# Kernel tuning notes

Hardware: AMD Instinct MI355X
Metric: run time of the kernel (lower is better)

## Reference

```python
import jax, jax.numpy as jnp
import numpy as np

B, D_IN, U, M = 8192, 512, 256, 50  # batch, input_size, num_units(=v_size), max_n_msgs


def _w(key, shape, scale=0.02):
    return (jax.random.normal(key, shape, dtype=jnp.float32) * scale)


def setup_inputs() -> dict:
    key = jax.random.key(0)
    ks = jax.random.split(key, 32)
    inp = {
        "X": jax.random.normal(ks[0], (B, D_IN), dtype=jnp.float32),
        "S": jax.random.normal(ks[1], (B, M, U), dtype=jnp.float32),
        "h": jax.random.normal(ks[2], (B, U), dtype=jnp.float32),
        "v": jax.random.normal(ks[3], (B, U), dtype=jnp.float32),
        # attention params
        "W_sa": _w(ks[4], (U, U)), "W_ha": _w(ks[5], (U, U)),
        "b_a": jnp.zeros((U,), jnp.float32), "v_a": _w(ks[6], (U,)),
        # gates
        "W_f": _w(ks[7], (U, U)), "W_hf": _w(ks[8], (U, U)), "b_f": jnp.zeros((U,), jnp.float32),
        "W_o": _w(ks[9], (U, U)), "W_ho": _w(ks[10], (U, U)), "b_o": jnp.zeros((U,), jnp.float32),
        "W_t": _w(ks[11], (U, U)), "W_ht": _w(ks[12], (U, U)), "b_t": jnp.zeros((U,), jnp.float32),
        "W_k": _w(ks[13], (D_IN, U)), "W_hk": _w(ks[14], (U, U)), "W_vk": _w(ks[15], (U, U)), "b_k": jnp.zeros((U,), jnp.float32),
        "W_s": _w(ks[16], (D_IN, U)), "W_hs": _w(ks[17], (U, U)), "b_s": jnp.zeros((U,), jnp.float32),
        "W_v": _w(ks[18], (U, U)), "W_hv": _w(ks[19], (U, U)), "b_v": jnp.zeros((U,), jnp.float32),
    }
    return inp


def reference(X, S, h, v,
              W_sa, W_ha, b_a, v_a,
              W_f, W_hf, b_f,
              W_o, W_ho, b_o,
              W_t, W_ht, b_t,
              W_k, W_hk, W_vk, b_k,
              W_s, W_hs, b_s,
              W_v, W_hv, b_v):
    # additive attention over messages: a [B, M, U]
    a = jnp.tanh(jnp.einsum('bmv,vu->bmu', S, W_sa) + (h @ W_ha + b_a)[:, None, :])
    scores = jnp.einsum('bmu,u->bm', a, v_a)            # [B, M]
    P = jax.nn.softmax(scores, axis=1)                  # [B, M]
    text = jnp.einsum('bm,bmv->bv', P, S)               # [B, U]
    # LSTM-like gates
    F = jax.nn.sigmoid(text @ W_f + h @ W_hf + b_f)
    O = jax.nn.sigmoid(text @ W_o + h @ W_ho + b_o)
    text_new = jnp.tanh(text @ W_t + h @ W_ht + b_t)
    V = F * v + O * text_new                            # [B, U]
    k = jax.nn.sigmoid(X @ W_k + h @ W_hk + V @ W_vk + b_k)
    hx = jnp.tanh(X @ W_s + h @ W_hs + b_s)
    hv = jnp.tanh(V @ W_v + h @ W_hv + b_v)
    H = (1.0 - k) * hv + k * hx                         # [B, U]
    # original returns (H, P, MSINStateTuple(H, V)); new_state.h == H
    return (H, P, V)
```

## Files before the change

kernel.cpp:

```cpp
#include <hip/hip_runtime.h>
#include <cstddef>

typedef __bf16 bf16x8 __attribute__((ext_vector_type(8)));
typedef unsigned short u16x8 __attribute__((ext_vector_type(8)));
typedef float f32x4 __attribute__((ext_vector_type(4)));

#define B_N 8192
#define M_N 50
#define R_N (B_N * M_N)
#define P_OFF ((size_t)B_N * 256)
#define V_OFF ((size_t)B_N * 256 + (size_t)B_N * 50)

__device__ __forceinline__ float bf2f(unsigned short u) {
  return __uint_as_float(((unsigned int)u) << 16);
}
__device__ __forceinline__ unsigned short f2bf(float f) {
  unsigned int u = __float_as_uint(f);
  u += 0x7fffu + ((u >> 16) & 1u);
  return (unsigned short)(u >> 16);
}
__device__ __forceinline__ float fsig(float x) { return 1.f / (1.f + __expf(-x)); }
__device__ __forceinline__ float ftanh(float x) {
  float e = __expf(2.f * x);
  return 1.f - 2.f / (e + 1.f);
}

__device__ __forceinline__ float ld_ext(const void* p, size_t i, bool f32) {
  return f32 ? ((const float*)p)[i] : bf2f(((const unsigned short*)p)[i]);
}
__device__ __forceinline__ void ld8_ext(unsigned short* dst, const void* p, size_t i, bool f32) {
  if (f32) {
    const float* fp = (const float*)p + i;
    const float4 a = *(const float4*)fp;
    const float4 b = *(const float4*)(fp + 4);
    u16x8 t;
    t[0] = f2bf(a.x); t[1] = f2bf(a.y); t[2] = f2bf(a.z); t[3] = f2bf(a.w);
    t[4] = f2bf(b.x); t[5] = f2bf(b.y); t[6] = f2bf(b.z); t[7] = f2bf(b.w);
    *(u16x8*)dst = t;
  } else {
    *(uint4*)dst = *(const uint4*)((const unsigned short*)p + i);
  }
}

__global__ void probe_dtype(const void* __restrict__ X, int* __restrict__ flag) {
  const int lane = threadIdx.x;
  const unsigned short u = ((const unsigned short*)X)[lane * 2];
  const int e = (u >> 7) & 0xff;
  const bool plausible = (e >= 110 && e <= 144) || (u == 0);
  const unsigned long long m = __ballot(plausible);
  if (lane == 0) *flag = (__popcll(m) < 32) ? 1 : 0;
}

struct TJobs {
  const void* src[15];
  unsigned short* dst[15];
  int K[15];
};

__global__ __launch_bounds__(256) void transpose_weights(TJobs jobs, const int* __restrict__ flagp) {
  const bool f32 = *flagp != 0;
  const int z = blockIdx.z;
  const void* __restrict__ src = jobs.src[z];
  unsigned short* __restrict__ dst = jobs.dst[z];
  const int K = jobs.K[z];
  const int k0 = blockIdx.y * 16;
  if (k0 >= K) return;
  const int n0 = blockIdx.x * 16;
  __shared__ __align__(16) unsigned short tile[16][17];
  const int tx = threadIdx.x & 15, ty = threadIdx.x >> 4;
  const size_t sidx = (size_t)(k0 + ty) * 256 + n0 + tx;
  tile[ty][tx] = f32 ? f2bf(((const float*)src)[sidx]) : ((const unsigned short*)src)[sidx];
  __syncthreads();
  dst[(size_t)(n0 + ty) * K + k0 + tx] = tile[tx][ty];
}

struct GJob {
  const void* A[3];
  const unsigned short* Wt[3];
  int K[3];
  int atag[3];
  const void* bias;
  const unsigned short* add;
  unsigned short* out;
  int act;
};
struct GJobs { GJob j[4]; };

__global__ __launch_bounds__(256) void gemm_small(GJobs jobs, const int* __restrict__ flagp) {
  const bool flag32 = *flagp != 0;
  const GJob job = jobs.j[blockIdx.z];
  const int tid = threadIdx.x;
  const int row0 = blockIdx.x * 64;
  const int col0 = blockIdx.y * 128;
  __shared__ __align__(16) unsigned short As[64][40];
  __shared__ __align__(16) unsigned short Ws[128][40];

  f32x4 acc[2][4];
#pragma unroll
  for (int i = 0; i < 2; ++i)
#pragma unroll
    for (int j = 0; j < 4; ++j) acc[i][j] = (f32x4){0.f, 0.f, 0.f, 0.f};

  const int wave = tid >> 6, lane = tid & 63;
  const int wr = wave >> 1, wc = wave & 1;
  const int quad = lane >> 4, l16 = lane & 15;

  for (int p = 0; p < 3; ++p) {
    const int Kp = job.K[p];
    if (Kp == 0) break;
    const void* __restrict__ Ap = job.A[p];
    const unsigned short* __restrict__ Wp = job.Wt[p];
    const bool af32 = (job.atag[p] == 1) || (job.atag[p] == 2 && flag32);
    for (int k0 = 0; k0 < Kp; k0 += 32) {
      {
        const int r = tid >> 2, c = (tid & 3) * 8;
        ld8_ext(&As[r][c], Ap, (size_t)(row0 + r) * Kp + k0 + c, af32);
      }
      for (int i = tid; i < 512; i += 256) {
        const int r = i >> 2, c = (i & 3) * 8;
        *(uint4*)&Ws[r][c] = *(const uint4*)&Wp[(size_t)(col0 + r) * Kp + k0 + c];
      }
      __syncthreads();
      bf16x8 af[2], bfr[4];
#pragma unroll
      for (int mi = 0; mi < 2; ++mi)
        af[mi] = *(const bf16x8*)&As[wr * 32 + mi * 16 + l16][quad * 8];
#pragma unroll
      for (int ni = 0; ni < 4; ++ni)
        bfr[ni] = *(const bf16x8*)&Ws[wc * 64 + ni * 16 + l16][quad * 8];
#pragma unroll
      for (int mi = 0; mi < 2; ++mi)
#pragma unroll
        for (int ni = 0; ni < 4; ++ni)
          acc[mi][ni] = __builtin_amdgcn_mfma_f32_16x16x32_bf16(af[mi], bfr[ni], acc[mi][ni], 0, 0, 0);
      __syncthreads();
    }
  }

#pragma unroll
  for (int mi = 0; mi < 2; ++mi) {
#pragma unroll
    for (int ni = 0; ni < 4; ++ni) {
      const int col = col0 + wc * 64 + ni * 16 + l16;
      const float bias = job.bias ? ld_ext(job.bias, col, flag32) : 0.f;
      const int rowb = row0 + wr * 32 + mi * 16 + quad * 4;
#pragma unroll
      for (int r = 0; r < 4; ++r) {
        float v = acc[mi][ni][r] + bias;
        const size_t idx = (size_t)(rowb + r) * 256 + col;
        if (job.add) v += bf2f(job.add[idx]);
        if (job.act == 1) v = fsig(v);
        else if (job.act == 2) v = ftanh(v);
        job.out[idx] = f2bf(v);
      }
    }
  }
}

__global__ __launch_bounds__(256) void attn_scores(
    const void* __restrict__ S,
    const unsigned short* __restrict__ WsaT,
    const unsigned short* __restrict__ hWa,
    const void* __restrict__ v_a,
    float* __restrict__ scores,
    const int* __restrict__ flagp) {
  const bool f32 = *flagp != 0;
  const int tid = threadIdx.x;
  const int r0 = blockIdx.x * 64;
  __shared__ __align__(16) unsigned short As[64][40];
  __shared__ __align__(16) unsigned short Ws[256][40];
  __shared__ float hWs[3][256];
  __shared__ float vas[256];
  __shared__ float red[64][4];

  const int b_first = r0 / 50;
  for (int i = tid; i < 768; i += 256) {
    const int j = i >> 8, u = i & 255;
    const int b = b_first + j;
    hWs[j][u] = (b < B_N) ? bf2f(hWa[(size_t)b * 256 + u]) : 0.f;
  }
  vas[tid] = ld_ext(v_a, tid, f32);

  f32x4 acc[4][4];
#pragma unroll
  for (int i = 0; i < 4; ++i)
#pragma unroll
    for (int j = 0; j < 4; ++j) acc[i][j] = (f32x4){0.f, 0.f, 0.f, 0.f};

  const int wave = tid >> 6, lane = tid & 63;
  const int quad = lane >> 4, l16 = lane & 15;

  for (int k0 = 0; k0 < 256; k0 += 32) {
    {
      const int r = tid >> 2, c = (tid & 3) * 8;
      ld8_ext(&As[r][c], S, (size_t)(r0 + r) * 256 + k0 + c, f32);
    }
    for (int i = tid; i < 1024; i += 256) {
      const int r = i >> 2, c = (i & 3) * 8;
      *(uint4*)&Ws[r][c] = *(const uint4*)&WsaT[(size_t)r * 256 + k0 + c];
    }
    __syncthreads();
    bf16x8 af[4], bfr[4];
#pragma unroll
    for (int mi = 0; mi < 4; ++mi)
      af[mi] = *(const bf16x8*)&As[mi * 16 + l16][quad * 8];
#pragma unroll
    for (int ni = 0; ni < 4; ++ni)
      bfr[ni] = *(const bf16x8*)&Ws[wave * 64 + ni * 16 + l16][quad * 8];
#pragma unroll
    for (int mi = 0; mi < 4; ++mi)
#pragma unroll
      for (int ni = 0; ni < 4; ++ni)
        acc[mi][ni] = __builtin_amdgcn_mfma_f32_16x16x32_bf16(af[mi], bfr[ni], acc[mi][ni], 0, 0, 0);
    __syncthreads();
  }

  float ps[4][4];
#pragma unroll
  for (int mi = 0; mi < 4; ++mi)
#pragma unroll
    for (int r = 0; r < 4; ++r) ps[mi][r] = 0.f;

#pragma unroll
  for (int mi = 0; mi < 4; ++mi) {
#pragma unroll
    for (int ni = 0; ni < 4; ++ni) {
      const int col = wave * 64 + ni * 16 + l16;
      const float va = vas[col];
#pragma unroll
      for (int r = 0; r < 4; ++r) {
        const int rowr = r0 + mi * 16 + quad * 4 + r;
        const int bj = rowr / 50 - b_first;
        ps[mi][r] += ftanh(acc[mi][ni][r] + hWs[bj][col]) * va;
      }
    }
  }
#pragma unroll
  for (int mi = 0; mi < 4; ++mi)
#pragma unroll
    for (int r = 0; r < 4; ++r) {
      float v = ps[mi][r];
      v += __shfl_xor(v, 1);
      v += __shfl_xor(v, 2);
      v += __shfl_xor(v, 4);
      v += __shfl_xor(v, 8);
      if (l16 == 0) red[mi * 16 + quad * 4 + r][wave] = v;
    }
  __syncthreads();
  if (tid < 64) scores[r0 + tid] = red[tid][0] + red[tid][1] + red[tid][2] + red[tid][3];
}

__global__ __launch_bounds__(256) void softmax_text(
    const float* __restrict__ scores,
    const void* __restrict__ S,
    float* __restrict__ out,
    unsigned short* __restrict__ text,
    const int* __restrict__ flagp) {
  const bool f32 = *flagp != 0;
  const int tid = threadIdx.x;
  const int wave = tid >> 6, lane = tid & 63;
  const int b = blockIdx.x * 4 + wave;
  __shared__ float Pl[4][64];

  float s = (lane < 50) ? scores[(size_t)b * 50 + lane] : -1e30f;
  float mx = s;
#pragma unroll
  for (int off = 32; off > 0; off >>= 1) mx = fmaxf(mx, __shfl_xor(mx, off));
  float e = (lane < 50) ? __expf(s - mx) : 0.f;
  float sum = e;
#pragma unroll
  for (int off = 32; off > 0; off >>= 1) sum += __shfl_xor(sum, off);
  const float p = e / sum;
  if (lane < 50) out[P_OFF + (size_t)b * 50 + lane] = p;
  Pl[wave][lane] = p;
  __syncthreads();

  float a0 = 0.f, a1 = 0.f, a2 = 0.f, a3 = 0.f;
  const size_t base = (size_t)b * 50 * 256 + lane * 4;
  for (int m = 0; m < 50; ++m) {
    const float pm = Pl[wave][m];
    const size_t ix = base + (size_t)m * 256;
    float s0, s1, s2, s3;
    if (f32) {
      const float4 sv = *(const float4*)((const float*)S + ix);
      s0 = sv.x; s1 = sv.y; s2 = sv.z; s3 = sv.w;
    } else {
      const uint2 raw = *(const uint2*)((const unsigned short*)S + ix);
      s0 = bf2f((unsigned short)(raw.x & 0xffffu));
      s1 = bf2f((unsigned short)(raw.x >> 16));
      s2 = bf2f((unsigned short)(raw.y & 0xffffu));
      s3 = bf2f((unsigned short)(raw.y >> 16));
    }
    a0 += pm * s0; a1 += pm * s1; a2 += pm * s2; a3 += pm * s3;
  }
  uint2 o;
  o.x = (unsigned int)f2bf(a0) | ((unsigned int)f2bf(a1) << 16);
  o.y = (unsigned int)f2bf(a2) | ((unsigned int)f2bf(a3) << 16);
  *(uint2*)&text[(size_t)b * 256 + lane * 4] = o;
}

__global__ __launch_bounds__(256) void v_combine(
    const unsigned short* __restrict__ F, const unsigned short* __restrict__ O,
    const unsigned short* __restrict__ T,
    const void* __restrict__ v, float* __restrict__ out,
    const int* __restrict__ flagp) {
  const bool f32 = *flagp != 0;
  const int i = (blockIdx.x * 256 + threadIdx.x) * 4;
  float v0, v1, v2, v3;
  if (f32) {
    const float4 vv = *(const float4*)((const float*)v + i);
    v0 = vv.x; v1 = vv.y; v2 = vv.z; v3 = vv.w;
  } else {
    const uint2 vr = *(const uint2*)((const unsigned short*)v + i);
    v0 = bf2f((unsigned short)(vr.x & 0xffffu));
    v1 = bf2f((unsigned short)(vr.x >> 16));
    v2 = bf2f((unsigned short)(vr.y & 0xffffu));
    v3 = bf2f((unsigned short)(vr.y >> 16));
  }
  const uint2 Fr = *(const uint2*)&F[i];
  const uint2 Or = *(const uint2*)&O[i];
  const uint2 Tr = *(const uint2*)&T[i];
  float4 o;
  o.x = bf2f((unsigned short)(Fr.x & 0xffffu)) * v0 + bf2f((unsigned short)(Or.x & 0xffffu)) * bf2f((unsigned short)(Tr.x & 0xffffu));
  o.y = bf2f((unsigned short)(Fr.x >> 16))     * v1 + bf2f((unsigned short)(Or.x >> 16))     * bf2f((unsigned short)(Tr.x >> 16));
  o.z = bf2f((unsigned short)(Fr.y & 0xffffu)) * v2 + bf2f((unsigned short)(Or.y & 0xffffu)) * bf2f((unsigned short)(Tr.y & 0xffffu));
  o.w = bf2f((unsigned short)(Fr.y >> 16))     * v3 + bf2f((unsigned short)(Or.y >> 16))     * bf2f((unsigned short)(Tr.y >> 16));
  *(float4*)&out[V_OFF + i] = o;
}

__global__ __launch_bounds__(256) void h_combine(
    const unsigned short* __restrict__ kk, const unsigned short* __restrict__ hv,
    const unsigned short* __restrict__ hx, float* __restrict__ Hout) {
  const int i = (blockIdx.x * 256 + threadIdx.x) * 4;
  const uint2 kr = *(const uint2*)&kk[i];
  const uint2 vr = *(const uint2*)&hv[i];
  const uint2 xr = *(const uint2*)&hx[i];
  const float k0 = bf2f((unsigned short)(kr.x & 0xffffu)), k1 = bf2f((unsigned short)(kr.x >> 16));
  const float k2 = bf2f((unsigned short)(kr.y & 0xffffu)), k3 = bf2f((unsigned short)(kr.y >> 16));
  const float hv0 = bf2f((unsigned short)(vr.x & 0xffffu)), hv1 = bf2f((unsigned short)(vr.x >> 16));
  const float hv2 = bf2f((unsigned short)(vr.y & 0xffffu)), hv3 = bf2f((unsigned short)(vr.y >> 16));
  const float hx0 = bf2f((unsigned short)(xr.x & 0xffffu)), hx1 = bf2f((unsigned short)(xr.x >> 16));
  const float hx2 = bf2f((unsigned short)(xr.y & 0xffffu)), hx3 = bf2f((unsigned short)(xr.y >> 16));
  float4 o;
  o.x = (1.f - k0) * hv0 + k0 * hx0;
  o.y = (1.f - k1) * hv1 + k1 * hx1;
  o.z = (1.f - k2) * hv2 + k2 * hx2;
  o.w = (1.f - k3) * hv3 + k3 * hx3;
  *(float4*)&Hout[i] = o;
}

extern "C" void kernel_launch(void* const* d_in, const int* in_sizes, int n_in,
                              void* d_out, int out_size, void* d_ws, size_t ws_size,
                              hipStream_t stream) {
  const void* X   = d_in[0];
  const void* S   = d_in[1];
  const void* h   = d_in[2];
  const void* v   = d_in[3];
  const void* b_a = d_in[6];
  const void* v_a = d_in[7];
  const void* b_f = d_in[10];
  const void* b_o = d_in[13];
  const void* b_t = d_in[16];
  const void* b_k = d_in[20];
  const void* b_s = d_in[23];
  const void* b_v = d_in[26];

  float* out = (float*)d_out;
  float* out_V = out + V_OFF;

  char* ws = (char*)d_ws;
  int* flag = (int*)ws;
  size_t off = 256;

  const int widx[15] = {4, 5, 8, 9, 11, 12, 14, 15, 17, 18, 19, 21, 22, 24, 25};
  const int wK[15]   = {256, 256, 256, 256, 256, 256, 256, 256, 512, 256, 256, 512, 256, 256, 256};
  TJobs tj;
  unsigned short* wt[15];
  for (int i = 0; i < 15; ++i) {
    wt[i] = (unsigned short*)(ws + off);
    off += (size_t)wK[i] * 256 * 2;
    tj.src[i] = d_in[widx[i]];
    tj.dst[i] = wt[i];
    tj.K[i] = wK[i];
  }
  const unsigned short *WsaT = wt[0], *WhaT = wt[1], *WfT = wt[2], *WhfT = wt[3],
                       *WoT = wt[4], *WhoT = wt[5], *WtT = wt[6], *WhtT = wt[7],
                       *WkT = wt[8], *WhkT = wt[9], *WvkT = wt[10], *WsT = wt[11],
                       *WhsT = wt[12], *WvT = wt[13], *WhvT = wt[14];
  off = (off + 255) & ~(size_t)255;
  const size_t BS = (size_t)B_N * 256 * 2;
  unsigned short* hWa   = (unsigned short*)(ws + off); off += BS;
  float* scores         = (float*)(ws + off);          off += (size_t)R_N * sizeof(float);
  unsigned short* text  = (unsigned short*)(ws + off); off += BS;
  unsigned short* Fb    = (unsigned short*)(ws + off); off += BS;
  unsigned short* Ob    = (unsigned short*)(ws + off); off += BS;
  unsigned short* Tb    = (unsigned short*)(ws + off); off += BS;
  unsigned short* kpre  = (unsigned short*)(ws + off); off += BS;
  unsigned short* hx    = (unsigned short*)(ws + off); off += BS;
  unsigned short* hvpre = (unsigned short*)(ws + off); off += BS;

  probe_dtype<<<1, 64, 0, stream>>>(X, flag);
  transpose_weights<<<dim3(16, 32, 15), 256, 0, stream>>>(tj, flag);

  GJobs jA;
  for (int i = 0; i < 4; ++i) jA.j[i] = GJob{};
  jA.j[0].A[0] = h;  jA.j[0].atag[0] = 2; jA.j[0].Wt[0] = WhaT; jA.j[0].K[0] = 256;
  jA.j[0].bias = b_a; jA.j[0].out = hWa; jA.j[0].act = 0;
  jA.j[1].A[0] = X;  jA.j[1].atag[0] = 2; jA.j[1].Wt[0] = WkT;  jA.j[1].K[0] = 512;
  jA.j[1].A[1] = h;  jA.j[1].atag[1] = 2; jA.j[1].Wt[1] = WhkT; jA.j[1].K[1] = 256;
  jA.j[1].bias = b_k; jA.j[1].out = kpre; jA.j[1].act = 0;
  jA.j[2].A[0] = X;  jA.j[2].atag[0] = 2; jA.j[2].Wt[0] = WsT;  jA.j[2].K[0] = 512;
  jA.j[2].A[1] = h;  jA.j[2].atag[1] = 2; jA.j[2].Wt[1] = WhsT; jA.j[2].K[1] = 256;
  jA.j[2].bias = b_s; jA.j[2].out = hx; jA.j[2].act = 2;
  jA.j[3].A[0] = h;  jA.j[3].atag[0] = 2; jA.j[3].Wt[0] = WhvT; jA.j[3].K[0] = 256;
  jA.j[3].bias = b_v; jA.j[3].out = hvpre; jA.j[3].act = 0;
  gemm_small<<<dim3(128, 2, 4), 256, 0, stream>>>(jA, flag);

  attn_scores<<<dim3(R_N / 64), 256, 0, stream>>>(S, WsaT, hWa, v_a, scores, flag);
  softmax_text<<<dim3(B_N / 4), 256, 0, stream>>>(scores, S, out, text, flag);

  GJobs jB;
  for (int i = 0; i < 4; ++i) jB.j[i] = GJob{};
  jB.j[0].A[0] = text; jB.j[0].atag[0] = 0; jB.j[0].Wt[0] = WfT;  jB.j[0].K[0] = 256;
  jB.j[0].A[1] = h;    jB.j[0].atag[1] = 2; jB.j[0].Wt[1] = WhfT; jB.j[0].K[1] = 256;
  jB.j[0].bias = b_f; jB.j[0].out = Fb; jB.j[0].act = 1;
  jB.j[1].A[0] = text; jB.j[1].atag[0] = 0; jB.j[1].Wt[0] = WoT;  jB.j[1].K[0] = 256;
  jB.j[1].A[1] = h;    jB.j[1].atag[1] = 2; jB.j[1].Wt[1] = WhoT; jB.j[1].K[1] = 256;
  jB.j[1].bias = b_o; jB.j[1].out = Ob; jB.j[1].act = 1;
  jB.j[2].A[0] = text; jB.j[2].atag[0] = 0; jB.j[2].Wt[0] = WtT;  jB.j[2].K[0] = 256;
  jB.j[2].A[1] = h;    jB.j[2].atag[1] = 2; jB.j[2].Wt[1] = WhtT; jB.j[2].K[1] = 256;
  jB.j[2].bias = b_t; jB.j[2].out = Tb; jB.j[2].act = 2;
  gemm_small<<<dim3(128, 2, 3), 256, 0, stream>>>(jB, flag);

  v_combine<<<dim3(B_N * 256 / 1024), 256, 0, stream>>>(Fb, Ob, Tb, v, out, flag);

  GJobs jC;
  for (int i = 0; i < 4; ++i) jC.j[i] = GJob{};
  jC.j[0].A[0] = out_V; jC.j[0].atag[0] = 1; jC.j[0].Wt[0] = WvkT; jC.j[0].K[0] = 256;
  jC.j[0].add = kpre; jC.j[0].out = kpre; jC.j[0].act = 1;
  jC.j[1].A[0] = out_V; jC.j[1].atag[0] = 1; jC.j[1].Wt[0] = WvT;  jC.j[1].K[0] = 256;
  jC.j[1].add = hvpre; jC.j[1].out = hvpre; jC.j[1].act = 2;
  gemm_small<<<dim3(128, 2, 2), 256, 0, stream>>>(jC, flag);

  h_combine<<<dim3(B_N * 256 / 1024), 256, 0, stream>>>(kpre, hvpre, hx, out);
}
```

Measured before the change: 924.2 us.

## Enlarge attention-score tiles, use direct global-to-LDS loads with XOR swizzle

The attention-score GEMM now uses 128-row tiles with 512 threads arranged as a 2x4 wave grid. This halves how often the Wsa weight tile is reloaded per row of S. Loads of bf16 S and of the weights go straight from global memory into LDS through global_load_lds, and an XOR swizzle replaces the padded shared layout to avoid bank conflicts. The change aims to cut the traffic and instruction overhead of staging through registers, at the cost of larger blocks, fewer blocks in flight, and a path that still converts f32 through registers.

Result: faster. 864.1 us (-6.5%).

```diff
diff --git a/kernel.cpp b/kernel.cpp
--- a/kernel.cpp
+++ b/kernel.cpp
@@ -40,6 +40,16 @@
   } else {
     *(uint4*)dst = *(const uint4*)((const unsigned short*)p + i);
   }
+}
+
+__device__ __forceinline__ void gload_lds16(const void* g, void* l) {
+  __builtin_amdgcn_global_load_lds(
+      (const __attribute__((address_space(1))) unsigned int*)g,
+      (__attribute__((address_space(3))) unsigned int*)l, 16, 0, 0);
+}
+
+__device__ __forceinline__ unsigned swz(unsigned b) {
+  return b ^ (((b >> 7) & 7u) << 4);
 }
 
 __global__ void probe_dtype(const void* __restrict__ X, int* __restrict__ flag) {
@@ -157,7 +167,7 @@
   }
 }
 
-__global__ __launch_bounds__(256) void attn_scores(
+__global__ __launch_bounds__(512, 4) void attn_scores(
     const void* __restrict__ S,
     const unsigned short* __restrict__ WsaT,
     const unsigned short* __restrict__ hWa,
@@ -166,20 +176,25 @@
     const int* __restrict__ flagp) {
   const bool f32 = *flagp != 0;
   const int tid = threadIdx.x;
-  const int r0 = blockIdx.x * 64;
-  __shared__ __align__(16) unsigned short As[64][40];
-  __shared__ __align__(16) unsigned short Ws[256][40];
-  __shared__ float hWs[3][256];
+  const int r0 = blockIdx.x * 128;
+
+  __shared__ __align__(128) unsigned short As[128 * 32];
+  __shared__ __align__(128) unsigned short Ws[256 * 32];
+  __shared__ float hWs[4][256];
   __shared__ float vas[256];
-  __shared__ float red[64][4];
+  __shared__ __align__(16) float red[128][4];
+
+  const int wave = tid >> 6, lane = tid & 63;
+  const int wr = wave >> 2, wc = wave & 3;
+  const int quad = lane >> 4, l16 = lane & 15;
 
   const int b_first = r0 / 50;
-  for (int i = tid; i < 768; i += 256) {
+  for (int i = tid; i < 1024; i += 512) {
     const int j = i >> 8, u = i & 255;
     const int b = b_first + j;
     hWs[j][u] = (b < B_N) ? bf2f(hWa[(size_t)b * 256 + u]) : 0.f;
   }
-  vas[tid] = ld_ext(v_a, tid, f32);
+  if (tid < 256) vas[tid] = ld_ext(v_a, tid, f32);
 
   f32x4 acc[4][4];
 #pragma unroll
@@ -187,26 +202,46 @@
 #pragma unroll
     for (int j = 0; j < 4; ++j) acc[i][j] = (f32x4){0.f, 0.f, 0.f, 0.f};
 
-  const int wave = tid >> 6, lane = tid & 63;
-  const int quad = lane >> 4, l16 = lane & 15;
+  const unsigned oA = tid * 16;
+  const unsigned lA = swz(oA);
+  const unsigned rowA = lA >> 6, slA = (lA >> 4) & 3;
+  const size_t gAbase = (size_t)(r0 + rowA) * 256 + slA * 8;
+  char* const ldsA = (char*)As + (wave << 10);
+
+  const unsigned lW0 = swz(tid * 16);
+  const unsigned rowW0 = lW0 >> 6, slW0 = (lW0 >> 4) & 3;
+  const unsigned lW1 = swz((tid + 512) * 16);
+  const unsigned rowW1 = lW1 >> 6, slW1 = (lW1 >> 4) & 3;
+  char* const ldsW0 = (char*)Ws + (wave << 10);
+  char* const ldsW1 = (char*)Ws + 8192 + (wave << 10);
 
   for (int k0 = 0; k0 < 256; k0 += 32) {
-    {
-      const int r = tid >> 2, c = (tid & 3) * 8;
-      ld8_ext(&As[r][c], S, (size_t)(r0 + r) * 256 + k0 + c, f32);
-    }
-    for (int i = tid; i < 1024; i += 256) {
-      const int r = i >> 2, c = (i & 3) * 8;
-      *(uint4*)&Ws[r][c] = *(const uint4*)&WsaT[(size_t)r * 256 + k0 + c];
-    }
+    if (f32) {
+      const float* fp = (const float*)S + gAbase + k0;
+      const float4 a = *(const float4*)fp;
+      const float4 b = *(const float4*)(fp + 4);
+      u16x8 t;
+      t[0] = f2bf(a.x); t[1] = f2bf(a.y); t[2] = f2bf(a.z); t[3] = f2bf(a.w);
+      t[4] = f2bf(b.x); t[5] = f2bf(b.y); t[6] = f2bf(b.z); t[7] = f2bf(b.w);
+      *(u16x8*)((char*)As + oA) = t;
+    } else {
+      gload_lds16((const unsigned short*)S + gAbase + k0, ldsA);
+    }
+    gload_lds16(WsaT + (size_t)rowW0 * 256 + k0 + slW0 * 8, ldsW0);
+    gload_lds16(WsaT + (size_t)rowW1 * 256 + k0 + slW1 * 8, ldsW1);
     __syncthreads();
+
     bf16x8 af[4], bfr[4];
 #pragma unroll
-    for (int mi = 0; mi < 4; ++mi)
-      af[mi] = *(const bf16x8*)&As[mi * 16 + l16][quad * 8];
-#pragma unroll
-    for (int ni = 0; ni < 4; ++ni)
-      bfr[ni] = *(const bf16x8*)&Ws[wave * 64 + ni * 16 + l16][quad * 8];
+    for (int mi = 0; mi < 4; ++mi) {
+      const unsigned lb = (unsigned)(wr * 64 + mi * 16 + l16) * 64 + quad * 16;
+      af[mi] = *(const bf16x8*)((const char*)As + swz(lb));
+    }
+#pragma unroll
+    for (int ni = 0; ni < 4; ++ni) {
+      const unsigned lb = (unsigned)(wc * 64 + ni * 16 + l16) * 64 + quad * 16;
+      bfr[ni] = *(const bf16x8*)((const char*)Ws + swz(lb));
+    }
 #pragma unroll
     for (int mi = 0; mi < 4; ++mi)
 #pragma unroll
@@ -217,22 +252,18 @@
 
   float ps[4][4];
 #pragma unroll
-  for (int mi = 0; mi < 4; ++mi)
-#pragma unroll
-    for (int r = 0; r < 4; ++r) ps[mi][r] = 0.f;
-
-#pragma unroll
   for (int mi = 0; mi < 4; ++mi) {
 #pragma unroll
-    for (int ni = 0; ni < 4; ++ni) {
-      const int col = wave * 64 + ni * 16 + l16;
-      const float va = vas[col];
-#pragma unroll
-      for (int r = 0; r < 4; ++r) {
-        const int rowr = r0 + mi * 16 + quad * 4 + r;
-        const int bj = rowr / 50 - b_first;
-        ps[mi][r] += ftanh(acc[mi][ni][r] + hWs[bj][col]) * va;
+    for (int r = 0; r < 4; ++r) {
+      const int rl = wr * 64 + mi * 16 + quad * 4 + r;
+      const int bj = (r0 + rl) / 50 - b_first;
+      float s = 0.f;
+#pragma unroll
+      for (int ni = 0; ni < 4; ++ni) {
+        const int col = wc * 64 + ni * 16 + l16;
+        s += ftanh(acc[mi][ni][r] + hWs[bj][col]) * vas[col];
       }
+      ps[mi][r] = s;
     }
   }
 #pragma unroll
@@ -244,10 +275,13 @@
       v += __shfl_xor(v, 2);
       v += __shfl_xor(v, 4);
       v += __shfl_xor(v, 8);
-      if (l16 == 0) red[mi * 16 + quad * 4 + r][wave] = v;
+      if (l16 == 0) red[wr * 64 + mi * 16 + quad * 4 + r][wc] = v;
     }
   __syncthreads();
-  if (tid < 64) scores[r0 + tid] = red[tid][0] + red[tid][1] + red[tid][2] + red[tid][3];
+  if (tid < 128) {
+    const float4 rr = *(const float4*)&red[tid][0];
+    scores[r0 + tid] = rr.x + rr.y + rr.z + rr.w;
+  }
 }
 
 __global__ __launch_bounds__(256) void softmax_text(
@@ -416,7 +450,7 @@
   jA.j[3].bias = b_v; jA.j[3].out = hvpre; jA.j[3].act = 0;
   gemm_small<<<dim3(128, 2, 4), 256, 0, stream>>>(jA, flag);
 
-  attn_scores<<<dim3(R_N / 64), 256, 0, stream>>>(S, WsaT, hWa, v_a, scores, flag);
+  attn_scores<<<dim3(R_N / 128), 512, 0, stream>>>(S, WsaT, hWa, v_a, scores, flag);
   softmax_text<<<dim3(B_N / 4), 256, 0, stream>>>(scores, S, out, text, flag);
 
   GJobs jB;
```
